# Optimization experiments

Hardware: AMD Instinct MI355X
Metric: run time of the kernel (lower is better)

## Reference

```python
import jax, jax.numpy as jnp
import numpy as np

N = 50000      # number of 'oa' nodes
E = 800000     # edges per metapath
IN_DIM = 128
OUT_DIM = 64   # per-head channels (concat=False -> mean over heads)
HEADS = 4
M = 3          # number of metapaths
NEG_SLOPE = 0.2  # PyG GATConv default leaky_relu slope


def setup_inputs() -> dict:
    key = jax.random.key(0)
    ks = jax.random.split(key, 32)
    inp = {"x": jax.random.normal(ks[0], (N, IN_DIM), jnp.float32)}
    for i in range(M):
        inp[f"edge_index_{i}"] = jax.random.randint(ks[1 + i], (2, E), 0, N, jnp.int32)
        inp[f"W_{i}"] = jax.random.normal(ks[4 + i], (IN_DIM, HEADS * OUT_DIM), jnp.float32) * (1.0 / np.sqrt(IN_DIM))
        inp[f"att_src_{i}"] = jax.random.normal(ks[7 + i], (HEADS, OUT_DIM), jnp.float32) * 0.1
        inp[f"att_dst_{i}"] = jax.random.normal(ks[10 + i], (HEADS, OUT_DIM), jnp.float32) * 0.1
        inp[f"bias_{i}"] = jnp.zeros((OUT_DIM,), jnp.float32)
    inp["proj_W"] = jax.random.normal(ks[20], (OUT_DIM, OUT_DIM), jnp.float32) * (1.0 / np.sqrt(OUT_DIM))
    inp["proj_b"] = jnp.zeros((OUT_DIM,), jnp.float32)
    inp["attn_vec"] = jax.random.normal(ks[21], (OUT_DIM,), jnp.float32) * 0.1
    return inp


def _gat_conv(x, edge_index, W, att_src, att_dst, bias):
    """PyG GATConv(in,out,heads,concat=False), eval mode, add_self_loops=True."""
    loop = jnp.arange(N, dtype=edge_index.dtype)
    src = jnp.concatenate([edge_index[0], loop])  # [E+N]
    dst = jnp.concatenate([edge_index[1], loop])
    h = (x @ W).reshape(N, HEADS, OUT_DIM)                 # [N,H,C]
    a_src = jnp.einsum('nhc,hc->nh', h, att_src)           # [N,H]
    a_dst = jnp.einsum('nhc,hc->nh', h, att_dst)
    e = jax.nn.leaky_relu(a_src[src] + a_dst[dst], NEG_SLOPE)  # [E+N,H]
    # edge softmax over incoming edges of each dst node (numerically stable)
    emax = jax.ops.segment_max(e, dst, num_segments=N)
    e = jnp.exp(e - emax[dst])
    denom = jax.ops.segment_sum(e, dst, num_segments=N)
    alpha = e / denom[dst]                                 # [E+N,H]; denom>0 via self loops
    out = jax.ops.segment_sum(h[src] * alpha[:, :, None], dst, num_segments=N)  # [N,H,C]
    return out.mean(axis=1) + bias                         # concat=False -> head mean


def reference(x, edge_index_0, edge_index_1, edge_index_2,
              W_0, W_1, W_2, att_src_0, att_src_1, att_src_2,
              att_dst_0, att_dst_1, att_dst_2, bias_0, bias_1, bias_2,
              proj_W, proj_b, attn_vec):
    eis = (edge_index_0, edge_index_1, edge_index_2)
    Ws = (W_0, W_1, W_2)
    a_s = (att_src_0, att_src_1, att_src_2)
    a_d = (att_dst_0, att_dst_1, att_dst_2)
    bs = (bias_0, bias_1, bias_2)
    z = [jax.nn.elu(_gat_conv(x, eis[i], Ws[i], a_s[i], a_d[i], bs[i])) for i in range(M)]
    z_stack = jnp.stack(z, axis=1)                          # [N,M,C]
    weights = jnp.tanh(z_stack @ proj_W + proj_b)           # [N,M,C]
    scores = jnp.einsum('nmc,c->nm', weights, attn_vec)     # [N,M]
    beta = jax.nn.softmax(scores, axis=1)                   # [N,M]
    z_final = jnp.einsum('nmc,nm->nc', z_stack, beta)       # [N,C]
    return z_final, beta
```

## Files before the change

kernel.cpp:

```cpp
#include <hip/hip_runtime.h>
#include <hip/hip_bf16.h>
#include <math.h>

#define NN 50000
#define EE 800000
#define IND 128
#define OUTD 64
#define NH 4
#define HC 256
#define WSZ 224
#define NWN 224
#define WCAP 4096
#define BATCH 2048
#define NBATCH ((EE + BATCH - 1) / BATCH)
#define PB (3 * NBATCH)
#define NMT 3125
#define CVTB 6250
#define WPB 48

typedef unsigned short u16;
typedef __attribute__((ext_vector_type(8))) short short8v;
typedef __attribute__((ext_vector_type(4))) float f32x4;
typedef __attribute__((ext_vector_type(2))) _Float16 half2v;

__device__ __forceinline__ float lrelu(float v) { return v > 0.f ? v : 0.2f * v; }
__device__ __forceinline__ u16 f2b(float f) {
  __hip_bfloat16 h = __float2bfloat16(f);
  return __builtin_bit_cast(u16, h);
}
__device__ __forceinline__ float b2f(u16 u) {
  return __uint_as_float((unsigned)u << 16);
}
__device__ __forceinline__ u16 f2h(float f) {
  _Float16 h = (_Float16)f;
  return __builtin_bit_cast(u16, h);
}
__device__ __forceinline__ float h2f(u16 u) {
  return (float)__builtin_bit_cast(_Float16, u);
}
__device__ __forceinline__ unsigned packh2(float a, float b) {
  half2v v = {(_Float16)a, (_Float16)b};
  return __builtin_bit_cast(unsigned, v);
}
__device__ __forceinline__ float dot2h(unsigned hpair, unsigned apair, float acc) {
#if __has_builtin(__builtin_amdgcn_fdot2)
  return __builtin_amdgcn_fdot2(__builtin_bit_cast(half2v, hpair),
                                __builtin_bit_cast(half2v, apair), acc, false);
#else
  acc = fmaf(h2f((u16)(hpair & 0xffff)), h2f((u16)(apair & 0xffff)), acc);
  return fmaf(h2f((u16)(hpair >> 16)), h2f((u16)(apair >> 16)), acc);
#endif
}

__global__ __launch_bounds__(256) void k_front(const int* __restrict__ ei0,
                                               const int* __restrict__ ei1,
                                               const int* __restrict__ ei2,
                                               int* __restrict__ gcur,
                                               unsigned int* __restrict__ glist,
                                               const float* __restrict__ x,
                                               u16* __restrict__ hi,
                                               u16* __restrict__ lo,
                                               const float* __restrict__ W0,
                                               const float* __restrict__ W1,
                                               const float* __restrict__ W2,
                                               const float* __restrict__ as0,
                                               const float* __restrict__ as1,
                                               const float* __restrict__ as2,
                                               const float* __restrict__ ad0,
                                               const float* __restrict__ ad1,
                                               const float* __restrict__ ad2,
                                               u16* __restrict__ wt,
                                               float* __restrict__ attS,
                                               float* __restrict__ attD) {
  __shared__ unsigned int stage[BATCH];
  __shared__ int cnt[NWN], strt[NWN], gbase[NWN];
  const int bx = blockIdx.x;
  const int tid = threadIdx.x;
  if (bx < PB) {
    const int m = bx / NBATCH;
    const int e0 = (bx - m * NBATCH) * BATCH;
    const int* ei = m == 0 ? ei0 : (m == 1 ? ei1 : ei2);
    if (tid < NWN) cnt[tid] = 0;
    __syncthreads();
    int bk[8], rk[8];
    unsigned int pk[8];
#pragma unroll
    for (int k = 0; k < 8; ++k) {
      const int e = e0 + k * 256 + tid;
      bk[k] = -1; rk[k] = 0; pk[k] = 0;
      if (e < EE) {
        const int d = ei[EE + e];
        const int s = ei[e];
        const int b = d / WSZ;
        bk[k] = b;
        pk[k] = ((unsigned)d << 16) | (unsigned)s;
        rk[k] = atomicAdd(&cnt[b], 1);
      }
    }
    __syncthreads();
    if (tid < 64) {
      const int base = tid * 4;
      int c0 = 0, c1 = 0, c2 = 0, c3 = 0;
      if (base + 0 < NWN) c0 = cnt[base + 0];
      if (base + 1 < NWN) c1 = cnt[base + 1];
      if (base + 2 < NWN) c2 = cnt[base + 2];
      if (base + 3 < NWN) c3 = cnt[base + 3];
      const int tot = c0 + c1 + c2 + c3;
      int run = tot;
#pragma unroll
      for (int off = 1; off < 64; off <<= 1) {
        const int u = __shfl_up(run, off, 64);
        if (tid >= off) run += u;
      }
      int ex = run - tot;
      if (base + 0 < NWN) { strt[base + 0] = ex; ex += c0; }
      if (base + 1 < NWN) { strt[base + 1] = ex; ex += c1; }
      if (base + 2 < NWN) { strt[base + 2] = ex; ex += c2; }
      if (base + 3 < NWN) { strt[base + 3] = ex; }
    }
    __syncthreads();
    if (tid < NWN && cnt[tid] > 0)
      gbase[tid] = atomicAdd(&gcur[m * NWN + tid], cnt[tid]);
#pragma unroll
    for (int k = 0; k < 8; ++k)
      if (bk[k] >= 0) stage[strt[bk[k]] + rk[k]] = pk[k];
    __syncthreads();
    const int unit = tid >> 3;
    const int l8 = tid & 7;
    for (int b = unit; b < NWN; b += 32) {
      const int len = cnt[b];
      if (len == 0) continue;
      const int st = strt[b];
      const int gb = gbase[b];
      unsigned int* dst = glist + (size_t)(m * NWN + b) * WCAP;
      for (int i = l8; i < len; i += 8)
        if (gb + i < WCAP) dst[gb + i] = stage[st + i];
    }
    return;
  }
  const int px = bx - PB;
  if (px < CVTB) {
    const int i = (px * 256 + tid) * 4;
    const float4 v = *(const float4*)(x + i);
    ushort4 h, l;
    h.x = f2b(v.x); l.x = f2b(v.x - b2f(h.x));
    h.y = f2b(v.y); l.y = f2b(v.y - b2f(h.y));
    h.z = f2b(v.z); l.z = f2b(v.z - b2f(h.z));
    h.w = f2b(v.w); l.w = f2b(v.w - b2f(h.w));
    *(ushort4*)(hi + i) = h;
    *(ushort4*)(lo + i) = l;
    return;
  }
  const int b = px - CVTB;
  const int m = b >> 4;
  const int kc = b & 15;
  const float* W = m == 0 ? W0 : (m == 1 ? W1 : W2);
  const int col = tid;
  const int colp = (col & 63) * 4 + (col >> 6);
#pragma unroll
  for (int kk = 0; kk < 8; ++kk) {
    const int k = kc * 8 + kk;
    wt[(size_t)m * (HC * IND) + colp * IND + k] = f2b(W[k * HC + col]);
  }
  if (kc == 0) {
    const float* as = m == 0 ? as0 : (m == 1 ? as1 : as2);
    const float* ad = m == 0 ? ad0 : (m == 1 ? ad1 : ad2);
    attS[m * HC + colp] = as[col];
    attD[m * HC + colp] = ad[col];
  }
}

__global__ __launch_bounds__(256) void k_sort(unsigned int* glist,
                                              const int* __restrict__ gcur,
                                              int* __restrict__ rowptr) {
  __shared__ u16 srt[WCAP];
  __shared__ int cnt[WSZ], row[WSZ + 1], cur[WSZ];
  const int m = blockIdx.y;
  const int w = blockIdx.x;
  const int tid = threadIdx.x;
  const int ne = min(gcur[m * NWN + w], WCAP);
  unsigned int* gl = glist + (size_t)(m * NWN + w) * WCAP;
  if (tid < WSZ) cnt[tid] = 0;
  __syncthreads();
  for (int i = tid; i < ne; i += 256)
    atomicAdd(&cnt[(int)(gl[i] >> 16) - w * WSZ], 1);
  __syncthreads();
  if (tid < 64) {
    const int base = tid * 4;
    int c0 = 0, c1 = 0, c2 = 0, c3 = 0;
    if (base + 0 < WSZ) c0 = cnt[base + 0];
    if (base + 1 < WSZ) c1 = cnt[base + 1];
    if (base + 2 < WSZ) c2 = cnt[base + 2];
    if (base + 3 < WSZ) c3 = cnt[base + 3];
    const int tot = c0 + c1 + c2 + c3;
    int run = tot;
#pragma unroll
    for (int off = 1; off < 64; off <<= 1) {
      const int u = __shfl_up(run, off, 64);
      if (tid >= off) run += u;
    }
    int ex = run - tot;
    if (base + 0 < WSZ) { row[base + 0] = ex; cur[base + 0] = ex; ex += c0; }
    if (base + 1 < WSZ) { row[base + 1] = ex; cur[base + 1] = ex; ex += c1; }
    if (base + 2 < WSZ) { row[base + 2] = ex; cur[base + 2] = ex; ex += c2; }
    if (base + 3 < WSZ) { row[base + 3] = ex; cur[base + 3] = ex; }
    if (tid == 63) row[WSZ] = ne;
  }
  __syncthreads();
  for (int i = tid; i < ne; i += 256) {
    const unsigned int v = gl[i];
    const int dl = (int)(v >> 16) - w * WSZ;
    const int p = atomicAdd(&cur[dl], 1);
    srt[p] = (u16)(v & 0xffffu);
  }
  __syncthreads();
  u16* cdst = (u16*)gl;
  for (int i = tid; i < ne; i += 256) cdst[i] = srt[i];
  int* rp = rowptr + (size_t)(m * NWN + w) * (WSZ + 1);
  if (tid <= WSZ) rp[tid] = row[tid];
}

__global__ __launch_bounds__(256) void k_mgemm(const u16* __restrict__ xhi,
                                               const u16* __restrict__ xlo,
                                               const u16* __restrict__ wtB,
                                               const float* __restrict__ attSB,
                                               const float* __restrict__ attDB,
                                               u16* __restrict__ H16B,
                                               float* __restrict__ a_srcB,
                                               float* __restrict__ a_dstB,
                                               int strideH, int strideA) {
  const int m = blockIdx.y;
  const u16* wt = wtB + (size_t)m * (HC * IND);
  const float* attS = attSB + m * HC;
  const float* attD = attDB + m * HC;
  u16* H16 = H16B + (size_t)m * strideH;
  float* a_src = a_srcB + (size_t)m * strideA;
  float* a_dst = a_dstB + (size_t)m * strideA;
  const int tid = threadIdx.x;
  const int wid = tid >> 6;
  const int l = tid & 63;
  const int l15 = l & 15;
  const int lq = l >> 4;
  const int mt = blockIdx.x * 4 + wid;
  if (mt >= NMT) return;
  const int m0 = mt * 16;
  const size_t abase = (size_t)(m0 + l15) * IND + lq * 8;
  const u16* pa = xhi + abase;
  const u16* pl = xlo + abase;
  const u16* pb = wt + l15 * IND + lq * 8;
  f32x4 acc[16];
#pragma unroll
  for (int nt = 0; nt < 16; ++nt) acc[nt] = (f32x4){0.f, 0.f, 0.f, 0.f};
#pragma unroll
  for (int ks = 0; ks < 4; ++ks) {
    const short8v ahi = *(const short8v*)(pa + ks * 32);
    const short8v alo = *(const short8v*)(pl + ks * 32);
#pragma unroll
    for (int nt = 0; nt < 16; nt += 2) {
      const short8v b0 = *(const short8v*)(pb + (nt + 0) * 16 * IND + ks * 32);
      const short8v b1 = *(const short8v*)(pb + (nt + 1) * 16 * IND + ks * 32);
      acc[nt]     = __builtin_amdgcn_mfma_f32_16x16x32_bf16(ahi, b0, acc[nt],     0, 0, 0);
      acc[nt + 1] = __builtin_amdgcn_mfma_f32_16x16x32_bf16(ahi, b1, acc[nt + 1], 0, 0, 0);
      acc[nt]     = __builtin_amdgcn_mfma_f32_16x16x32_bf16(alo, b0, acc[nt],     0, 0, 0);
      acc[nt + 1] = __builtin_amdgcn_mfma_f32_16x16x32_bf16(alo, b1, acc[nt + 1], 0, 0, 0);
    }
  }
#pragma unroll
  for (int nt = 0; nt < 16; ++nt) {
#pragma unroll
    for (int r = 0; r < 4; ++r)
      H16[(size_t)(m0 + lq * 4 + r) * HC + nt * 16 + l15] = f2h(acc[nt][r]);
  }
  float asv[16], adv[16];
#pragma unroll
  for (int nt = 0; nt < 16; ++nt) {
    asv[nt] = attS[nt * 16 + l15];
    adv[nt] = attD[nt * 16 + l15];
  }
#pragma unroll
  for (int r = 0; r < 4; ++r) {
    float ps = 0.f, pd = 0.f;
#pragma unroll
    for (int nt = 0; nt < 16; ++nt) {
      ps = fmaf(acc[nt][r], asv[nt], ps);
      pd = fmaf(acc[nt][r], adv[nt], pd);
    }
    ps += __shfl_xor(ps, 4, 64); ps += __shfl_xor(ps, 8, 64);
    pd += __shfl_xor(pd, 4, 64); pd += __shfl_xor(pd, 8, 64);
    if (l15 < 4) {
      const int n = m0 + lq * 4 + r;
      a_src[n * NH + l15] = ps;
      a_dst[n * NH + l15] = pd;
    }
  }
}

__global__ __launch_bounds__(256) void k_aggr(const unsigned int* __restrict__ glistB,
                                              const int* __restrict__ rowptrB,
                                              const u16* __restrict__ H16B,
                                              const float* __restrict__ a_srcB,
                                              const float* __restrict__ a_dstB,
                                              const float* __restrict__ b0_,
                                              const float* __restrict__ b1_,
                                              const float* __restrict__ b2_,
                                              u16* __restrict__ zbB,
                                              int strideH, int strideA) {
  __shared__ uint4 slot[4][64];
  const int m = blockIdx.y;
  const unsigned int* glist_m = glistB + (size_t)m * NWN * WCAP;
  const int* rowptrm = rowptrB + (size_t)m * NWN * (WSZ + 1);
  const u16* H16 = H16B + (size_t)m * strideH;
  const float* a_src = a_srcB + (size_t)m * strideA;
  const float* a_dst = a_dstB + (size_t)m * strideA;
  const float* bias = m == 0 ? b0_ : (m == 1 ? b1_ : b2_);
  u16* zb = zbB + (size_t)m * NN * OUTD;
  const int wid = threadIdx.x >> 6;
  const int c = threadIdx.x & 63;
  const int d = blockIdx.x * 4 + wid;
  const int w = d / WSZ;
  const int dl = d - w * WSZ;
  const int* rp = rowptrm + (size_t)w * (WSZ + 1);
  const int r0 = rp[dl];
  const int nb = min(rp[dl + 1] - r0, 64);
  const u16* cw = (const u16*)(glist_m + (size_t)w * WCAP);
  const float4 adv = *(const float4*)&a_dst[d * NH];
  float4 evr = make_float4(0.f, 0.f, 0.f, 0.f);
  int sj = 0;
  if (c < nb) {
    sj = cw[r0 + c];
    const float4 asv = *(const float4*)&a_src[sj * NH];
    evr.x = __expf(lrelu(asv.x + adv.x));
    evr.y = __expf(lrelu(asv.y + adv.y));
    evr.z = __expf(lrelu(asv.z + adv.z));
    evr.w = __expf(lrelu(asv.w + adv.w));
  }
  float den0 = evr.x, den1 = evr.y, den2 = evr.z, den3 = evr.w;
#pragma unroll
  for (int mk = 32; mk; mk >>= 1) {
    den0 += __shfl_xor(den0, mk, 64);
    den1 += __shfl_xor(den1, mk, 64);
    den2 += __shfl_xor(den2, mk, 64);
    den3 += __shfl_xor(den3, mk, 64);
  }
  const float4 asl = *(const float4*)&a_src[d * NH];
  const float e0s = __expf(lrelu(asl.x + adv.x));
  const float e1s = __expf(lrelu(asl.y + adv.y));
  const float e2s = __expf(lrelu(asl.z + adv.z));
  const float e3s = __expf(lrelu(asl.w + adv.w));
  den0 += e0s; den1 += e1s; den2 += e2s; den3 += e3s;
  const float rd0 = 0.25f * __builtin_amdgcn_rcpf(den0);
  const float rd1 = 0.25f * __builtin_amdgcn_rcpf(den1);
  const float rd2 = 0.25f * __builtin_amdgcn_rcpf(den2);
  const float rd3 = 0.25f * __builtin_amdgcn_rcpf(den3);
  if (c < nb) {
    uint4 sv;
    sv.x = packh2(evr.x * rd0, evr.y * rd1);
    sv.y = packh2(evr.z * rd2, evr.w * rd3);
    sv.z = (unsigned)(sj * (HC * 2));
    sv.w = 0;
    slot[wid][c] = sv;
  }
  const ushort4 hs = *(const ushort4*)&H16[(size_t)d * HC + c * 4];
  float res = e0s * rd0 * h2f(hs.x);
  res = fmaf(e1s * rd1, h2f(hs.y), res);
  res = fmaf(e2s * rd2, h2f(hs.z), res);
  res = fmaf(e3s * rd3, h2f(hs.w), res);
  const unsigned char* Hb = (const unsigned char*)H16;
  const int c8 = c * 8;
  float accA = 0.f, accB = 0.f, accC = 0.f, accD = 0.f;
  int j = 0;
  for (; j + 4 <= nb; j += 4) {
    const uint4 sa = slot[wid][j + 0];
    const uint4 sb = slot[wid][j + 1];
    const uint4 sc = slot[wid][j + 2];
    const uint4 sd = slot[wid][j + 3];
    const uint2 ha = *(const uint2*)(Hb + (size_t)sa.z + c8);
    const uint2 hb = *(const uint2*)(Hb + (size_t)sb.z + c8);
    const uint2 hc = *(const uint2*)(Hb + (size_t)sc.z + c8);
    const uint2 hd = *(const uint2*)(Hb + (size_t)sd.z + c8);
    accA = dot2h(ha.x, sa.x, accA); accA = dot2h(ha.y, sa.y, accA);
    accB = dot2h(hb.x, sb.x, accB); accB = dot2h(hb.y, sb.y, accB);
    accC = dot2h(hc.x, sc.x, accC); accC = dot2h(hc.y, sc.y, accC);
    accD = dot2h(hd.x, sd.x, accD); accD = dot2h(hd.y, sd.y, accD);
  }
  for (; j < nb; ++j) {
    const uint4 sa = slot[wid][j];
    const uint2 ha = *(const uint2*)(Hb + (size_t)sa.z + c8);
    accA = dot2h(ha.x, sa.x, accA);
    accA = dot2h(ha.y, sa.y, accA);
  }
  res += (accA + accB) + (accC + accD);
  res += bias[c];
  res = res > 0.f ? res : __expf(res) - 1.f;
  zb[(size_t)d * OUTD + c] = f2b(res);
}

__global__ __launch_bounds__(256) void k_sem(const u16* __restrict__ zb,
                                             const float* __restrict__ proj_W,
                                             const float* __restrict__ proj_b,
                                             const float* __restrict__ attn_vec,
                                             float* __restrict__ out) {
  __shared__ float pw[64 * 64];
  __shared__ float zl[3][16][OUTD];
  const int tid = threadIdx.x;
  const int n0 = blockIdx.x * 16;
  for (int i = tid; i < 1024; i += 256)
    ((float4*)pw)[i] = ((const float4*)proj_W)[i];
#pragma unroll
  for (int mm = 0; mm < 3; ++mm) {
    const ushort4 v = ((const ushort4*)(zb + ((size_t)mm * NN + n0) * OUTD))[tid];
    float4 f;
    f.x = b2f(v.x); f.y = b2f(v.y); f.z = b2f(v.z); f.w = b2f(v.w);
    *(float4*)&zl[mm][tid >> 4][(tid & 15) * 4] = f;
  }
  __syncthreads();
  const int wid = tid >> 6;
  const int c = tid & 63;
  const float pb = proj_b[c];
  const float av = attn_vec[c];
  for (int nl = 0; nl < 4; ++nl) {
    const int node = wid * 4 + nl;
    float s[3];
#pragma unroll
    for (int mm = 0; mm < 3; ++mm) {
      float a0 = pb, a1 = 0.f, a2 = 0.f, a3 = 0.f;
#pragma unroll
      for (int kk = 0; kk < 16; ++kk) {
        a0 = fmaf(zl[mm][node][kk],      pw[kk * 64 + c],        a0);
        a1 = fmaf(zl[mm][node][16 + kk], pw[(16 + kk) * 64 + c], a1);
        a2 = fmaf(zl[mm][node][32 + kk], pw[(32 + kk) * 64 + c], a2);
        a3 = fmaf(zl[mm][node][48 + kk], pw[(48 + kk) * 64 + c], a3);
      }
      float xx = (a0 + a1) + (a2 + a3);
      xx = fminf(xx, 40.f);
      const float t = __expf(2.f * xx);
      const float th = (t - 1.f) * __builtin_amdgcn_rcpf(t + 1.f);
      float p = th * av;
#pragma unroll
      for (int mk = 32; mk; mk >>= 1) p += __shfl_xor(p, mk, 64);
      s[mm] = p;
    }
    const float mx = fmaxf(s[0], fmaxf(s[1], s[2]));
    const float e0 = __expf(s[0] - mx), e1 = __expf(s[1] - mx), e2 = __expf(s[2] - mx);
    const float inv = 1.0f / (e0 + e1 + e2);
    const float b0 = e0 * inv, b1 = e1 * inv, b2 = e2 * inv;
    const int n = n0 + node;
    const float zf = zl[0][node][c] * b0 + zl[1][node][c] * b1 + zl[2][node][c] * b2;
    out[(size_t)n * OUTD + c] = zf;
    if (c < 3) out[(size_t)NN * OUTD + n * 3 + c] = (c == 0 ? b0 : (c == 1 ? b1 : b2));
  }
}

extern "C" void kernel_launch(void* const* d_in, const int* in_sizes, int n_in,
                              void* d_out, int out_size, void* d_ws, size_t ws_size,
                              hipStream_t stream) {
  const float* x = (const float*)d_in[0];
  const int* ei[3];
  const float* W[3];
  const float* as[3];
  const float* ad[3];
  const float* bs[3];

  if (in_sizes[2] != 2 * EE) {
    for (int m = 0; m < 3; ++m) {
      ei[m] = (const int*)d_in[1 + 5 * m];
      W[m]  = (const float*)d_in[2 + 5 * m];
      as[m] = (const float*)d_in[3 + 5 * m];
      ad[m] = (const float*)d_in[4 + 5 * m];
      bs[m] = (const float*)d_in[5 + 5 * m];
    }
  } else {
    for (int m = 0; m < 3; ++m) {
      ei[m] = (const int*)d_in[1 + m];
      W[m]  = (const float*)d_in[4 + m];
      as[m] = (const float*)d_in[7 + m];
      ad[m] = (const float*)d_in[10 + m];
      bs[m] = (const float*)d_in[13 + m];
    }
  }
  const float* proj_W = (const float*)d_in[16];
  const float* proj_b = (const float*)d_in[17];
  const float* attn_vec = (const float*)d_in[18];

  const bool batched = (ws_size >= (size_t)139000000);
  const int nrep = batched ? 3 : 1;

  char* ws = (char*)d_ws;
  size_t off = 0;
  u16* x16hi = (u16*)(ws + off);                     off += (size_t)NN * IND * 2;
  u16* x16lo = (u16*)(ws + off);                     off += (size_t)NN * IND * 2;
  u16* H16 = (u16*)(ws + off);                       off += (size_t)nrep * NN * HC * 2;
  u16* zb = (u16*)(ws + off);                        off += (size_t)3 * NN * OUTD * 2;
  float* a_srcb = (float*)(ws + off);                off += (size_t)nrep * NN * NH * 4;
  float* a_dstb = (float*)(ws + off);                off += (size_t)nrep * NN * NH * 4;
  int* gcur = (int*)(ws + off);                      off += (size_t)3 * NWN * 4;
  unsigned int* glist = (unsigned int*)(ws + off);   off += (size_t)3 * NWN * WCAP * 4;
  int* rowptr = (int*)(ws + off);                    off += (size_t)3 * NWN * (WSZ + 1) * 4;
  u16* wt16 = (u16*)(ws + off);                      off += (size_t)3 * HC * IND * 2;
  float* attSp = (float*)(ws + off);                 off += (size_t)3 * HC * 4;
  float* attDp = (float*)(ws + off);                 off += (size_t)3 * HC * 4;

  float* outp = (float*)d_out;

  hipMemsetAsync(gcur, 0, (size_t)3 * NWN * sizeof(int), stream);
  k_front<<<PB + CVTB + WPB, 256, 0, stream>>>(ei[0], ei[1], ei[2], gcur, glist,
                                               x, x16hi, x16lo,
                                               W[0], W[1], W[2], as[0], as[1], as[2],
                                               ad[0], ad[1], ad[2], wt16, attSp, attDp);
  k_sort<<<dim3(NWN, 3), 256, 0, stream>>>(glist, gcur, rowptr);

  if (batched) {
    k_mgemm<<<dim3((NMT + 3) / 4, 3), 256, 0, stream>>>(
        x16hi, x16lo, wt16, attSp, attDp, H16, a_srcb, a_dstb, NN * HC, NN * NH);
    k_aggr<<<dim3(NN / 4, 3), 256, 0, stream>>>(
        glist, rowptr, H16, a_srcb, a_dstb, bs[0], bs[1], bs[2], zb, NN * HC, NN * NH);
  } else {
    for (int m = 0; m < 3; ++m) {
      k_mgemm<<<dim3((NMT + 3) / 4, 1), 256, 0, stream>>>(
          x16hi, x16lo, wt16 + (size_t)m * HC * IND, attSp + m * HC, attDp + m * HC,
          H16, a_srcb, a_dstb, 0, 0);
      k_aggr<<<dim3(NN / 4, 1), 256, 0, stream>>>(
          glist + (size_t)m * NWN * WCAP, rowptr + (size_t)m * NWN * (WSZ + 1),
          H16, a_srcb, a_dstb, bs[m], bs[m], bs[m],
          zb + (size_t)m * NN * OUTD, 0, 0);
    }
  }
  k_sem<<<NN / 16, 256, 0, stream>>>(zb, proj_W, proj_b, attn_vec, outp);
}
```

Before: 343.0 us.

## Fuse sort and GEMM into one launch, double GEMM rows, register proj_W

The CSR sort kernel and the projection GEMM are merged into one kernel launch: the first blocks do the per-window sort and the rest compute H, so the two independent stages share one grid and one launch. Each GEMM wave now computes 32 rows instead of 16, reusing each loaded B fragment for two A tiles to halve W traffic, at the cost of more accumulator registers. The semantic-attention kernel keeps its proj_W column in registers instead of shared memory and reads z as float4, which raises register pressure.

```diff
diff --git a/kernel.cpp b/kernel.cpp
--- a/kernel.cpp
+++ b/kernel.cpp
@@ -14,9 +14,11 @@
 #define BATCH 2048
 #define NBATCH ((EE + BATCH - 1) / BATCH)
 #define PB (3 * NBATCH)
-#define NMT 3125
 #define CVTB 6250
 #define WPB 48
+#define SORTB (3 * NWN)
+#define NMT2 1563
+#define MGB 391
 
 typedef unsigned short u16;
 typedef __attribute__((ext_vector_type(8))) short short8v;
@@ -170,106 +172,126 @@
   }
 }
 
-__global__ __launch_bounds__(256) void k_sort(unsigned int* glist,
-                                              const int* __restrict__ gcur,
-                                              int* __restrict__ rowptr) {
+__global__ __launch_bounds__(256) void k_mid(unsigned int* glist,
+                                             const int* __restrict__ gcur,
+                                             int* __restrict__ rowptr,
+                                             const u16* __restrict__ xhi,
+                                             const u16* __restrict__ xlo,
+                                             const u16* __restrict__ wtB,
+                                             const float* __restrict__ attSB,
+                                             const float* __restrict__ attDB,
+                                             u16* __restrict__ H16B,
+                                             float* __restrict__ a_srcB,
+                                             float* __restrict__ a_dstB,
+                                             int nsort, int mbase,
+                                             int strideH, int strideA) {
   __shared__ u16 srt[WCAP];
   __shared__ int cnt[WSZ], row[WSZ + 1], cur[WSZ];
-  const int m = blockIdx.y;
-  const int w = blockIdx.x;
+  const int bx = blockIdx.x;
   const int tid = threadIdx.x;
-  const int ne = min(gcur[m * NWN + w], WCAP);
-  unsigned int* gl = glist + (size_t)(m * NWN + w) * WCAP;
-  if (tid < WSZ) cnt[tid] = 0;
-  __syncthreads();
-  for (int i = tid; i < ne; i += 256)
-    atomicAdd(&cnt[(int)(gl[i] >> 16) - w * WSZ], 1);
-  __syncthreads();
-  if (tid < 64) {
-    const int base = tid * 4;
-    int c0 = 0, c1 = 0, c2 = 0, c3 = 0;
-    if (base + 0 < WSZ) c0 = cnt[base + 0];
-    if (base + 1 < WSZ) c1 = cnt[base + 1];
-    if (base + 2 < WSZ) c2 = cnt[base + 2];
-    if (base + 3 < WSZ) c3 = cnt[base + 3];
-    const int tot = c0 + c1 + c2 + c3;
-    int run = tot;
-#pragma unroll
-    for (int off = 1; off < 64; off <<= 1) {
-      const int u = __shfl_up(run, off, 64);
-      if (tid >= off) run += u;
-    }
-    int ex = run - tot;
-    if (base + 0 < WSZ) { row[base + 0] = ex; cur[base + 0] = ex; ex += c0; }
-    if (base + 1 < WSZ) { row[base + 1] = ex; cur[base + 1] = ex; ex += c1; }
-    if (base + 2 < WSZ) { row[base + 2] = ex; cur[base + 2] = ex; ex += c2; }
-    if (base + 3 < WSZ) { row[base + 3] = ex; cur[base + 3] = ex; }
-    if (tid == 63) row[WSZ] = ne;
-  }
-  __syncthreads();
-  for (int i = tid; i < ne; i += 256) {
-    const unsigned int v = gl[i];
-    const int dl = (int)(v >> 16) - w * WSZ;
-    const int p = atomicAdd(&cur[dl], 1);
-    srt[p] = (u16)(v & 0xffffu);
-  }
-  __syncthreads();
-  u16* cdst = (u16*)gl;
-  for (int i = tid; i < ne; i += 256) cdst[i] = srt[i];
-  int* rp = rowptr + (size_t)(m * NWN + w) * (WSZ + 1);
-  if (tid <= WSZ) rp[tid] = row[tid];
-}
-
-__global__ __launch_bounds__(256) void k_mgemm(const u16* __restrict__ xhi,
-                                               const u16* __restrict__ xlo,
-                                               const u16* __restrict__ wtB,
-                                               const float* __restrict__ attSB,
-                                               const float* __restrict__ attDB,
-                                               u16* __restrict__ H16B,
-                                               float* __restrict__ a_srcB,
-                                               float* __restrict__ a_dstB,
-                                               int strideH, int strideA) {
-  const int m = blockIdx.y;
-  const u16* wt = wtB + (size_t)m * (HC * IND);
-  const float* attS = attSB + m * HC;
-  const float* attD = attDB + m * HC;
-  u16* H16 = H16B + (size_t)m * strideH;
-  float* a_src = a_srcB + (size_t)m * strideA;
-  float* a_dst = a_dstB + (size_t)m * strideA;
-  const int tid = threadIdx.x;
+  if (bx < nsort) {
+    const int m = bx / NWN;
+    const int w = bx - m * NWN;
+    const int ne = min(gcur[m * NWN + w], WCAP);
+    unsigned int* gl = glist + (size_t)(m * NWN + w) * WCAP;
+    if (tid < WSZ) cnt[tid] = 0;
+    __syncthreads();
+    for (int i = tid; i < ne; i += 256)
+      atomicAdd(&cnt[(int)(gl[i] >> 16) - w * WSZ], 1);
+    __syncthreads();
+    if (tid < 64) {
+      const int base = tid * 4;
+      int c0 = 0, c1 = 0, c2 = 0, c3 = 0;
+      if (base + 0 < WSZ) c0 = cnt[base + 0];
+      if (base + 1 < WSZ) c1 = cnt[base + 1];
+      if (base + 2 < WSZ) c2 = cnt[base + 2];
+      if (base + 3 < WSZ) c3 = cnt[base + 3];
+      const int tot = c0 + c1 + c2 + c3;
+      int run = tot;
+#pragma unroll
+      for (int off = 1; off < 64; off <<= 1) {
+        const int u = __shfl_up(run, off, 64);
+        if (tid >= off) run += u;
+      }
+      int ex = run - tot;
+      if (base + 0 < WSZ) { row[base + 0] = ex; cur[base + 0] = ex; ex += c0; }
+      if (base + 1 < WSZ) { row[base + 1] = ex; cur[base + 1] = ex; ex += c1; }
+      if (base + 2 < WSZ) { row[base + 2] = ex; cur[base + 2] = ex; ex += c2; }
+      if (base + 3 < WSZ) { row[base + 3] = ex; cur[base + 3] = ex; }
+      if (tid == 63) row[WSZ] = ne;
+    }
+    __syncthreads();
+    for (int i = tid; i < ne; i += 256) {
+      const unsigned int v = gl[i];
+      const int dl = (int)(v >> 16) - w * WSZ;
+      const int p = atomicAdd(&cur[dl], 1);
+      srt[p] = (u16)(v & 0xffffu);
+    }
+    __syncthreads();
+    u16* cdst = (u16*)gl;
+    for (int i = tid; i < ne; i += 256) cdst[i] = srt[i];
+    int* rp = rowptr + (size_t)(m * NWN + w) * (WSZ + 1);
+    if (tid <= WSZ) rp[tid] = row[tid];
+    return;
+  }
+  const int b2 = bx - nsort;
+  const int m = mbase + b2 / MGB;
+  const int tg = b2 - (b2 / MGB) * MGB;
   const int wid = tid >> 6;
   const int l = tid & 63;
   const int l15 = l & 15;
   const int lq = l >> 4;
-  const int mt = blockIdx.x * 4 + wid;
-  if (mt >= NMT) return;
-  const int m0 = mt * 16;
-  const size_t abase = (size_t)(m0 + l15) * IND + lq * 8;
-  const u16* pa = xhi + abase;
-  const u16* pl = xlo + abase;
+  const int mt = tg * 4 + wid;
+  if (mt >= NMT2) return;
+  const int m0 = mt * 32;
+  const bool up = (m0 + 16 < NN);
+  const u16* wt = wtB + (size_t)(m - mbase) * 0 + (size_t)m * (HC * IND);
+  const float* attS = attSB + m * HC;
+  const float* attD = attDB + m * HC;
+  u16* H16 = H16B + (size_t)(m - mbase) * strideH;
+  float* a_src = a_srcB + (size_t)(m - mbase) * strideA;
+  float* a_dst = a_dstB + (size_t)(m - mbase) * strideA;
+  const size_t aA = (size_t)(m0 + l15) * IND + lq * 8;
+  const size_t aB = aA + (size_t)16 * IND;
   const u16* pb = wt + l15 * IND + lq * 8;
-  f32x4 acc[16];
-#pragma unroll
-  for (int nt = 0; nt < 16; ++nt) acc[nt] = (f32x4){0.f, 0.f, 0.f, 0.f};
+  f32x4 accA[16], accB[16];
+#pragma unroll
+  for (int nt = 0; nt < 16; ++nt) {
+    accA[nt] = (f32x4){0.f, 0.f, 0.f, 0.f};
+    accB[nt] = (f32x4){0.f, 0.f, 0.f, 0.f};
+  }
 #pragma unroll
   for (int ks = 0; ks < 4; ++ks) {
-    const short8v ahi = *(const short8v*)(pa + ks * 32);
-    const short8v alo = *(const short8v*)(pl + ks * 32);
-#pragma unroll
-    for (int nt = 0; nt < 16; nt += 2) {
-      const short8v b0 = *(const short8v*)(pb + (nt + 0) * 16 * IND + ks * 32);
-      const short8v b1 = *(const short8v*)(pb + (nt + 1) * 16 * IND + ks * 32);
-      acc[nt]     = __builtin_amdgcn_mfma_f32_16x16x32_bf16(ahi, b0, acc[nt],     0, 0, 0);
-      acc[nt + 1] = __builtin_amdgcn_mfma_f32_16x16x32_bf16(ahi, b1, acc[nt + 1], 0, 0, 0);
-      acc[nt]     = __builtin_amdgcn_mfma_f32_16x16x32_bf16(alo, b0, acc[nt],     0, 0, 0);
-      acc[nt + 1] = __builtin_amdgcn_mfma_f32_16x16x32_bf16(alo, b1, acc[nt + 1], 0, 0, 0);
+    const short8v a0h = *(const short8v*)(xhi + aA + ks * 32);
+    const short8v a0l = *(const short8v*)(xlo + aA + ks * 32);
+    short8v a1h = (short8v){0,0,0,0,0,0,0,0};
+    short8v a1l = (short8v){0,0,0,0,0,0,0,0};
+    if (up) {
+      a1h = *(const short8v*)(xhi + aB + ks * 32);
+      a1l = *(const short8v*)(xlo + aB + ks * 32);
+    }
+#pragma unroll
+    for (int nt = 0; nt < 16; ++nt) {
+      const short8v b0 = *(const short8v*)(pb + nt * 16 * IND + ks * 32);
+      accA[nt] = __builtin_amdgcn_mfma_f32_16x16x32_bf16(a0h, b0, accA[nt], 0, 0, 0);
+      accA[nt] = __builtin_amdgcn_mfma_f32_16x16x32_bf16(a0l, b0, accA[nt], 0, 0, 0);
+      accB[nt] = __builtin_amdgcn_mfma_f32_16x16x32_bf16(a1h, b0, accB[nt], 0, 0, 0);
+      accB[nt] = __builtin_amdgcn_mfma_f32_16x16x32_bf16(a1l, b0, accB[nt], 0, 0, 0);
     }
   }
 #pragma unroll
   for (int nt = 0; nt < 16; ++nt) {
 #pragma unroll
     for (int r = 0; r < 4; ++r)
-      H16[(size_t)(m0 + lq * 4 + r) * HC + nt * 16 + l15] = f2h(acc[nt][r]);
+      H16[(size_t)(m0 + lq * 4 + r) * HC + nt * 16 + l15] = f2h(accA[nt][r]);
+  }
+  if (up) {
+#pragma unroll
+    for (int nt = 0; nt < 16; ++nt) {
+#pragma unroll
+      for (int r = 0; r < 4; ++r)
+        H16[(size_t)(m0 + 16 + lq * 4 + r) * HC + nt * 16 + l15] = f2h(accB[nt][r]);
+    }
   }
   float asv[16], adv[16];
 #pragma unroll
@@ -279,18 +301,26 @@
   }
 #pragma unroll
   for (int r = 0; r < 4; ++r) {
-    float ps = 0.f, pd = 0.f;
+    float ps = 0.f, pd = 0.f, ps2 = 0.f, pd2 = 0.f;
 #pragma unroll
     for (int nt = 0; nt < 16; ++nt) {
-      ps = fmaf(acc[nt][r], asv[nt], ps);
-      pd = fmaf(acc[nt][r], adv[nt], pd);
+      ps = fmaf(accA[nt][r], asv[nt], ps);
+      pd = fmaf(accA[nt][r], adv[nt], pd);
+      ps2 = fmaf(accB[nt][r], asv[nt], ps2);
+      pd2 = fmaf(accB[nt][r], adv[nt], pd2);
     }
     ps += __shfl_xor(ps, 4, 64); ps += __shfl_xor(ps, 8, 64);
     pd += __shfl_xor(pd, 4, 64); pd += __shfl_xor(pd, 8, 64);
+    ps2 += __shfl_xor(ps2, 4, 64); ps2 += __shfl_xor(ps2, 8, 64);
+    pd2 += __shfl_xor(pd2, 4, 64); pd2 += __shfl_xor(pd2, 8, 64);
     if (l15 < 4) {
       const int n = m0 + lq * 4 + r;
       a_src[n * NH + l15] = ps;
       a_dst[n * NH + l15] = pd;
+      if (up) {
+        a_src[(n + 16) * NH + l15] = ps2;
+        a_dst[(n + 16) * NH + l15] = pd2;
+      }
     }
   }
 }
@@ -304,14 +334,14 @@
                                               const float* __restrict__ b1_,
                                               const float* __restrict__ b2_,
                                               u16* __restrict__ zbB,
-                                              int strideH, int strideA) {
+                                              int mbase, int strideH, int strideA) {
   __shared__ uint4 slot[4][64];
-  const int m = blockIdx.y;
+  const int m = mbase + blockIdx.y;
   const unsigned int* glist_m = glistB + (size_t)m * NWN * WCAP;
   const int* rowptrm = rowptrB + (size_t)m * NWN * (WSZ + 1);
-  const u16* H16 = H16B + (size_t)m * strideH;
-  const float* a_src = a_srcB + (size_t)m * strideA;
-  const float* a_dst = a_dstB + (size_t)m * strideA;
+  const u16* H16 = H16B + (size_t)blockIdx.y * strideH;
+  const float* a_src = a_srcB + (size_t)blockIdx.y * strideA;
+  const float* a_dst = a_dstB + (size_t)blockIdx.y * strideA;
   const float* bias = m == 0 ? b0_ : (m == 1 ? b1_ : b2_);
   u16* zb = zbB + (size_t)m * NN * OUTD;
   const int wid = threadIdx.x >> 6;
@@ -400,12 +430,14 @@
                                              const float* __restrict__ proj_b,
                                              const float* __restrict__ attn_vec,
                                              float* __restrict__ out) {
-  __shared__ float pw[64 * 64];
   __shared__ float zl[3][16][OUTD];
   const int tid = threadIdx.x;
   const int n0 = blockIdx.x * 16;
-  for (int i = tid; i < 1024; i += 256)
-    ((float4*)pw)[i] = ((const float4*)proj_W)[i];
+  const int wid = tid >> 6;
+  const int c = tid & 63;
+  float pwc[64];
+#pragma unroll
+  for (int k = 0; k < 64; ++k) pwc[k] = proj_W[k * OUTD + c];
 #pragma unroll
   for (int mm = 0; mm < 3; ++mm) {
     const ushort4 v = ((const ushort4*)(zb + ((size_t)mm * NN + n0) * OUTD))[tid];
@@ -414,8 +446,6 @@
     *(float4*)&zl[mm][tid >> 4][(tid & 15) * 4] = f;
   }
   __syncthreads();
-  const int wid = tid >> 6;
-  const int c = tid & 63;
   const float pb = proj_b[c];
   const float av = attn_vec[c];
   for (int nl = 0; nl < 4; ++nl) {
@@ -423,13 +453,30 @@
     float s[3];
 #pragma unroll
     for (int mm = 0; mm < 3; ++mm) {
+      const float4* zr = (const float4*)&zl[mm][node][0];
       float a0 = pb, a1 = 0.f, a2 = 0.f, a3 = 0.f;
 #pragma unroll
-      for (int kk = 0; kk < 16; ++kk) {
-        a0 = fmaf(zl[mm][node][kk],      pw[kk * 64 + c],        a0);
-        a1 = fmaf(zl[mm][node][16 + kk], pw[(16 + kk) * 64 + c], a1);
-        a2 = fmaf(zl[mm][node][32 + kk], pw[(32 + kk) * 64 + c], a2);
-        a3 = fmaf(zl[mm][node][48 + kk], pw[(48 + kk) * 64 + c], a3);
+      for (int kq = 0; kq < 4; ++kq) {
+        const float4 z0 = zr[kq * 4 + 0];
+        const float4 z1 = zr[kq * 4 + 1];
+        const float4 z2 = zr[kq * 4 + 2];
+        const float4 z3 = zr[kq * 4 + 3];
+        a0 = fmaf(z0.x, pwc[kq * 16 + 0], a0);
+        a0 = fmaf(z0.y, pwc[kq * 16 + 1], a0);
+        a0 = fmaf(z0.z, pwc[kq * 16 + 2], a0);
+        a0 = fmaf(z0.w, pwc[kq * 16 + 3], a0);
+        a1 = fmaf(z1.x, pwc[kq * 16 + 4], a1);
+        a1 = fmaf(z1.y, pwc[kq * 16 + 5], a1);
+        a1 = fmaf(z1.z, pwc[kq * 16 + 6], a1);
+        a1 = fmaf(z1.w, pwc[kq * 16 + 7], a1);
+        a2 = fmaf(z2.x, pwc[kq * 16 + 8], a2);
+        a2 = fmaf(z2.y, pwc[kq * 16 + 9], a2);
+        a2 = fmaf(z2.z, pwc[kq * 16 + 10], a2);
+        a2 = fmaf(z2.w, pwc[kq * 16 + 11], a2);
+        a3 = fmaf(z3.x, pwc[kq * 16 + 12], a3);
+        a3 = fmaf(z3.y, pwc[kq * 16 + 13], a3);
+        a3 = fmaf(z3.z, pwc[kq * 16 + 14], a3);
+        a3 = fmaf(z3.w, pwc[kq * 16 + 15], a3);
       }
       float xx = (a0 + a1) + (a2 + a3);
       xx = fminf(xx, 40.f);
@@ -507,22 +554,29 @@
                                                x, x16hi, x16lo,
                                                W[0], W[1], W[2], as[0], as[1], as[2],
                                                ad[0], ad[1], ad[2], wt16, attSp, attDp);
-  k_sort<<<dim3(NWN, 3), 256, 0, stream>>>(glist, gcur, rowptr);
 
   if (batched) {
-    k_mgemm<<<dim3((NMT + 3) / 4, 3), 256, 0, stream>>>(
-        x16hi, x16lo, wt16, attSp, attDp, H16, a_srcb, a_dstb, NN * HC, NN * NH);
+    k_mid<<<SORTB + 3 * MGB, 256, 0, stream>>>(glist, gcur, rowptr,
+                                               x16hi, x16lo, wt16, attSp, attDp,
+                                               H16, a_srcb, a_dstb,
+                                               SORTB, 0, NN * HC, NN * NH);
     k_aggr<<<dim3(NN / 4, 3), 256, 0, stream>>>(
-        glist, rowptr, H16, a_srcb, a_dstb, bs[0], bs[1], bs[2], zb, NN * HC, NN * NH);
+        glist, rowptr, H16, a_srcb, a_dstb, bs[0], bs[1], bs[2], zb,
+        0, NN * HC, NN * NH);
   } else {
-    for (int m = 0; m < 3; ++m) {
-      k_mgemm<<<dim3((NMT + 3) / 4, 1), 256, 0, stream>>>(
-          x16hi, x16lo, wt16 + (size_t)m * HC * IND, attSp + m * HC, attDp + m * HC,
-          H16, a_srcb, a_dstb, 0, 0);
+    k_mid<<<SORTB + MGB, 256, 0, stream>>>(glist, gcur, rowptr,
+                                           x16hi, x16lo, wt16, attSp, attDp,
+                                           H16, a_srcb, a_dstb,
+                                           SORTB, 0, 0, 0);
+    k_aggr<<<dim3(NN / 4, 1), 256, 0, stream>>>(
+        glist, rowptr, H16, a_srcb, a_dstb, bs[0], bs[1], bs[2], zb, 0, 0, 0);
+    for (int m = 1; m < 3; ++m) {
+      k_mid<<<MGB, 256, 0, stream>>>(glist, gcur, rowptr,
+                                     x16hi, x16lo, wt16, attSp, attDp,
+                                     H16, a_srcb, a_dstb,
+                                     0, m, 0, 0);
       k_aggr<<<dim3(NN / 4, 1), 256, 0, stream>>>(
-          glist + (size_t)m * NWN * WCAP, rowptr + (size_t)m * NWN * (WSZ + 1),
-          H16, a_srcb, a_dstb, bs[m], bs[m], bs[m],
-          zb + (size_t)m * NN * OUTD, 0, 0);
+          glist, rowptr, H16, a_srcb, a_dstb, bs[0], bs[1], bs[2], zb, m, 0, 0);
     }
   }
   k_sem<<<NN / 16, 256, 0, stream>>>(zb, proj_W, proj_b, attn_vec, outp);
```

After: 320.1 us. -6.7%, faster.
